# Optimization experiments

Hardware: AMD Instinct MI355X
Metric: run time of the kernel (lower is better)

The kernel has to match this reference:

```python
import jax, jax.numpy as jnp
import numpy as np

NJ = 24
COL = 14
TMP = 3  # gaussian half-window (tmp_size)


def _forward(o, h, o3D, h3D, t, t3D, v):
    B = h.shape[0]
    f32 = jnp.float32
    scale = 1.0 / COL
    cc = COL * COL

    # ---- 2D heatmap argmax decode: x[i,j] = offset at argmax + coord*scale ----
    am = jnp.argmax(h.reshape(B, NJ, cc), axis=-1)            # (B, Nj)
    y2 = am // COL
    x2 = am % COL
    of = o.reshape(B, 2 * NJ, cc)
    gx = jnp.take_along_axis(of[:, :NJ], am[..., None], axis=-1)[..., 0]
    gy = jnp.take_along_axis(of[:, NJ:], am[..., None], axis=-1)[..., 0]
    x2d = jnp.stack([gx + x2.astype(f32) * scale,
                     gy + y2.astype(f32) * scale], axis=-1)   # (B, Nj, 2)

    # ---- 3D heatmap argmax decode ----
    h3r = h3D.reshape(B, NJ, COL, COL, COL)                   # (B, Nj, z, y, x)
    am3 = jnp.argmax(h3r.reshape(B, NJ, COL ** 3), axis=-1)
    z3 = am3 // cc
    r3 = am3 % cc
    y3 = r3 // COL
    x3 = r3 % COL
    o3r = o3D.reshape(B, 3, NJ, COL ** 3)                     # 3 coord channels
    g0 = jnp.take_along_axis(o3r[:, 0], am3[..., None], axis=-1)[..., 0]
    g1 = jnp.take_along_axis(o3r[:, 1], am3[..., None], axis=-1)[..., 0]
    g2 = jnp.take_along_axis(o3r[:, 2], am3[..., None], axis=-1)[..., 0]
    x3d = jnp.stack([g0 + x3.astype(f32) * scale,
                     g1 + y3.astype(f32) * scale,
                     g2 + (z3 - 7).astype(f32) * scale], axis=-1)  # (B, Nj, 3)

    v0 = v[..., 0]
    vis = (v0 == 1)

    # ---- 2D gaussian target placement (torch int() == floor for t >= 0) ----
    mu_x = jnp.floor(t[..., 0] * COL + 0.5).astype(jnp.int32)
    mu_y = jnp.floor(t[..., 1] * COL + 0.5).astype(jnp.int32)
    valid2d = ~((mu_x - TMP >= COL) | (mu_y - TMP >= COL) |
                (mu_x + TMP + 1 <= 0) | (mu_y + TMP + 1 <= 0))
    coords = jnp.arange(COL, dtype=jnp.int32)
    dx = coords[None, None, :] - mu_x[..., None]              # (B, Nj, COL)
    dy = coords[None, None, :] - mu_y[..., None]
    in2 = (jnp.abs(dx) <= TMP)[:, :, None, :] & (jnp.abs(dy) <= TMP)[:, :, :, None]
    sq2 = (dx.astype(f32) ** 2)[:, :, None, :] + (dy.astype(f32) ** 2)[:, :, :, None]
    gate2 = (vis & valid2d)[..., None, None]
    tt = jnp.where(in2 & gate2, jnp.exp(-0.5 * sq2), 0.0)     # (B, Nj, COL, COL)

    # ---- 3D gaussian target placement (only checked when still visible) ----
    m3x = jnp.floor(t3D[..., 0] * COL + 0.5).astype(jnp.int32)
    m3y = jnp.floor(t3D[..., 1] * COL + 0.5).astype(jnp.int32)
    m3z = jnp.floor(t3D[..., 2] * COL + 7 + 0.5).astype(jnp.int32)
    valid3d = ~((m3x - TMP >= COL) | (m3y - TMP >= COL) | (m3z - TMP >= COL) |
                (m3x + TMP + 1 < 0) | (m3y + TMP + 1 < 0) | (m3z + TMP + 1 < 0))
    dX = coords[None, None, :] - m3x[..., None]
    dY = coords[None, None, :] - m3y[..., None]
    dZ = coords[None, None, :] - m3z[..., None]
    in3 = ((jnp.abs(dX) <= TMP)[:, :, None, None, :] &
           (jnp.abs(dY) <= TMP)[:, :, None, :, None] &
           (jnp.abs(dZ) <= TMP)[:, :, :, None, None])
    sq3 = ((dX.astype(f32) ** 2)[:, :, None, None, :] +
           (dY.astype(f32) ** 2)[:, :, None, :, None] +
           (dZ.astype(f32) ** 2)[:, :, :, None, None])
    vf_bool = vis & valid2d & valid3d                          # final visibility
    tt3 = jnp.where(in3 & vf_bool[..., None, None, None], jnp.exp(-0.5 * sq3), 0.0)

    # ---- visibility mutation: v zeroed when a visible joint's target is OOB ----
    keep = jnp.where(vis, valid2d & valid3d, True)
    v_f = v * keep[..., None].astype(f32)                      # (B, Nj, 3)
    # x3D was skipped (left 0) when the 2D check invalidated a visible joint
    x3d = x3d * (~(vis & ~valid2d))[..., None].astype(f32)

    vf0 = v_f[..., 0]
    jmask = (vf0 != 0).astype(f32)                             # (B, Nj)
    cnt = jnp.sum(jmask)
    Nv = jnp.sum(v_f) / 3.0

    diff1 = (h - tt) * jmask[..., None, None]
    d1 = jnp.sqrt(jnp.sum(diff1 * diff1)) / cnt

    diff2 = (x2d - t) * v_f[..., :2]
    d2 = jnp.sqrt(jnp.sum(diff2 * diff2)) / Nv

    diff3 = (h3r - tt3) * jmask[..., None, None, None]
    d3 = jnp.sqrt(jnp.sum(diff3 * diff3)) / cnt

    diff4 = (x3d - t3D) * v_f
    d4 = jnp.sqrt(jnp.sum(diff4 * diff4)) / Nv

    return d1 + d2 + d3 + d4


def setup_inputs() -> dict:
    B = 256
    key = jax.random.key(0)
    ks = jax.random.split(key, 7)
    o = 0.1 * jax.random.normal(ks[0], (B, 2 * NJ, COL, COL), jnp.float32)
    h = jax.random.normal(ks[1], (B, NJ, COL, COL), jnp.float32)
    o3D = 0.1 * jax.random.normal(ks[2], (B, 3 * NJ * COL, COL, COL), jnp.float32)
    h3D = jax.random.normal(ks[3], (B, NJ * COL, COL, COL), jnp.float32)
    t = jax.random.uniform(ks[4], (B, NJ, 2), jnp.float32)
    t3D = jax.random.uniform(ks[5], (B, NJ, 3), jnp.float32)
    v0 = jax.random.bernoulli(ks[6], 0.8, (B, NJ)).astype(jnp.float32)
    v = jnp.repeat(v0[..., None], 3, axis=-1)
    return {"o": o, "h": h, "o3D": o3D, "h3D": h3D, "t": t, "t3D": t3D,
            "v": v, "d": 0, "path": 0}


def reference(o, h, o3D, h3D, t, t3D, v, d, path):
    # d > -990 selects the full d1+d2+d3+d4 loss (static Python branch)
    return _forward(o, h, o3D, h3D, t, t3D, v)
```

## Files before the change

kernel.cpp:

```cpp
#include <hip/hip_runtime.h>
#include <float.h>
#include <math.h>

#define NJ   24
#define COL  14
#define CC   196
#define CC3  2744
#define NV4_3D 686
#define NV4_2D 49
#define TMPW 3
#define PPB  4

__global__ __launch_bounds__(256)
void msed_pair_kernel(const float* __restrict__ o,
                      const float* __restrict__ h,
                      const float* __restrict__ o3D,
                      const float* __restrict__ h3D,
                      const float* __restrict__ t,
                      const float* __restrict__ t3D,
                      const float* __restrict__ v,
                      float* __restrict__ part,
                      int npairs)
{
    const int wv   = threadIdx.x >> 6;
    const int lane = threadIdx.x & 63;
    const int pair = blockIdx.x * PPB + wv;

    __shared__ float warr[PPB][6];

    float p0 = 0.f, p1 = 0.f, p2 = 0.f, p3 = 0.f, p4 = 0.f, p5 = 0.f;

    if (pair < npairs) {
        const float tx  = t[pair * 2 + 0];
        const float ty  = t[pair * 2 + 1];
        const float t3x = t3D[pair * 3 + 0];
        const float t3y = t3D[pair * 3 + 1];
        const float t3z = t3D[pair * 3 + 2];
        const float v0  = v[pair * 3 + 0];
        const float v1  = v[pair * 3 + 1];
        const float v2c = v[pair * 3 + 2];
        const bool vis = (v0 == 1.0f);

        const int mux = (int)floorf(tx * (float)COL + 0.5f);
        const int muy = (int)floorf(ty * (float)COL + 0.5f);
        const bool valid2d = !((mux - TMPW >= COL) || (muy - TMPW >= COL) ||
                               (mux + TMPW + 1 <= 0) || (muy + TMPW + 1 <= 0));

        const int m3x = (int)floorf(t3x * (float)COL + 0.5f);
        const int m3y = (int)floorf(t3y * (float)COL + 0.5f);
        const int m3z = (int)floorf(t3z * (float)COL + 7.0f + 0.5f);
        const bool valid3d = !((m3x - TMPW >= COL) || (m3y - TMPW >= COL) || (m3z - TMPW >= COL) ||
                               (m3x + TMPW + 1 < 0) || (m3y + TMPW + 1 < 0) || (m3z + TMPW + 1 < 0));

        const float keep = vis ? ((valid2d && valid3d) ? 1.0f : 0.0f) : 1.0f;
        const float vf0 = v0 * keep, vf1 = v1 * keep, vf2 = v2c * keep;
        const bool jm     = (vf0 != 0.0f);
        const bool active = jm || (vf1 != 0.0f) || (vf2 != 0.0f);
        const bool gate2  = vis && valid2d;
        const bool gate3  = vis && valid2d && valid3d;

        if (active) {
            const float4* hp3 = (const float4*)(h3D + (size_t)pair * CC3);
            float s3 = 0.0f;
            float bv3 = -FLT_MAX; int bi3 = 0x7FFFFFFF;
            #pragma unroll
            for (int u = 0; u < 11; ++u) {
                const int i = lane + (u << 6);
                const bool valid = (u < 10) || (lane < (NV4_3D - 640));
                const int ic = valid ? i : lane;
                float4 q = hp3[ic];
                float vals[4] = {q.x, q.y, q.z, q.w};
                const int e0 = ic * 4;
                #pragma unroll
                for (int c = 0; c < 4; ++c) {
                    float hv = vals[c];
                    if (valid) {
                        s3 += hv * hv;
                        if (hv > bv3) { bv3 = hv; bi3 = e0 + c; }
                    }
                }
            }

            float s1 = 0.0f;
            float bv2 = -FLT_MAX; int bi2 = 0x7FFFFFFF;
            if (lane < NV4_2D) {
                const float4* hp2 = (const float4*)(h + (size_t)pair * CC);
                float4 q = hp2[lane];
                float vals[4] = {q.x, q.y, q.z, q.w};
                const int e0 = lane * 4;
                #pragma unroll
                for (int c = 0; c < 4; ++c) {
                    float hv = vals[c];
                    s1 += hv * hv;
                    if (hv > bv2) { bv2 = hv; bi2 = e0 + c; }
                }
            }

            if (lane < 49) {
                const int dx = lane % 7 - TMPW;
                const int dy = lane / 7 - TMPW;
                const float gxy = __expf(-0.5f * (float)(dx * dx + dy * dy));

                if (gate2) {
                    const int x = mux + dx, y = muy + dy;
                    if ((unsigned)x < COL && (unsigned)y < COL) {
                        const float wh = h[(size_t)pair * CC + y * COL + x];
                        s1 += gxy * (gxy - 2.0f * wh);
                    }
                }
                if (gate3) {
                    const int x = m3x + dx, y = m3y + dy;
                    if ((unsigned)x < COL && (unsigned)y < COL) {
                        const float* base = h3D + (size_t)pair * CC3 + y * COL + x;
                        #pragma unroll
                        for (int dz = -TMPW; dz <= TMPW; ++dz) {
                            const int z = m3z + dz;
                            if ((unsigned)z < COL) {
                                const float g = gxy * __expf(-0.5f * (float)(dz * dz));
                                const float wh = base[z * CC];
                                s3 += g * (g - 2.0f * wh);
                            }
                        }
                    }
                }
            }

            #pragma unroll
            for (int off = 32; off > 0; off >>= 1) {
                s3 += __shfl_down(s3, off);
                s1 += __shfl_down(s1, off);
                float ov = __shfl_down(bv3, off); int oi = __shfl_down(bi3, off);
                if (ov > bv3 || (ov == bv3 && oi < bi3)) { bv3 = ov; bi3 = oi; }
                float ow = __shfl_down(bv2, off); int oj = __shfl_down(bi2, off);
                if (ow > bv2 || (ow == bv2 && oj < bi2)) { bv2 = ow; bi2 = oj; }
            }

            if (lane == 0) {
                const int b = pair / NJ;
                const int j = pair - b * NJ;
                const float scale = 1.0f / (float)COL;

                const int am = bi2;
                const int x2 = am % COL, y2 = am / COL;
                float gx = o[((size_t)b * (2 * NJ) + j) * CC + am];
                float gy = o[((size_t)b * (2 * NJ) + NJ + j) * CC + am];
                float x2dx = gx + (float)x2 * scale;
                float x2dy = gy + (float)y2 * scale;

                const int am3 = bi3;
                const int z3 = am3 / CC; const int r3 = am3 - z3 * CC;
                const int y3 = r3 / COL; const int x3 = r3 - y3 * COL;
                size_t base3 = (size_t)b * (3 * NJ * CC3) + (size_t)j * CC3 + am3;
                float g0 = o3D[base3];
                float g1 = o3D[base3 + (size_t)NJ * CC3];
                float g2 = o3D[base3 + (size_t)(2 * NJ) * CC3];
                float x3dx = g0 + (float)x3 * scale;
                float x3dy = g1 + (float)y3 * scale;
                float x3dz = g2 + (float)(z3 - 7) * scale;
                if (vis && !valid2d) { x3dx = 0.f; x3dy = 0.f; x3dz = 0.f; }

                float d2x = (x2dx - tx) * vf0;
                float d2y = (x2dy - ty) * vf1;
                float s2 = d2x * d2x + d2y * d2y;

                float d4x = (x3dx - t3x) * vf0;
                float d4y = (x3dy - t3y) * vf1;
                float d4z = (x3dz - t3z) * vf2;
                float s4 = d4x * d4x + d4y * d4y + d4z * d4z;

                p0 = jm ? s1 : 0.f;
                p1 = s2;
                p2 = jm ? s3 : 0.f;
                p3 = s4;
                p4 = jm ? 1.0f : 0.0f;
                p5 = vf0 + vf1 + vf2;
            }
        }
    }

    if (lane == 0) {
        warr[wv][0] = p0; warr[wv][1] = p1; warr[wv][2] = p2;
        warr[wv][3] = p3; warr[wv][4] = p4; warr[wv][5] = p5;
    }
    __syncthreads();

    if (threadIdx.x == 0) {
        float b0 = ((warr[0][0] + warr[1][0]) + warr[2][0]) + warr[3][0];
        float b1 = ((warr[0][1] + warr[1][1]) + warr[2][1]) + warr[3][1];
        float b2 = ((warr[0][2] + warr[1][2]) + warr[2][2]) + warr[3][2];
        float b3 = ((warr[0][3] + warr[1][3]) + warr[2][3]) + warr[3][3];
        float b4 = ((warr[0][4] + warr[1][4]) + warr[2][4]) + warr[3][4];
        float b5 = ((warr[0][5] + warr[1][5]) + warr[2][5]) + warr[3][5];
        *(float4*)(part + (size_t)blockIdx.x * 8)     = make_float4(b0, b1, b2, b3);
        *(float4*)(part + (size_t)blockIdx.x * 8 + 4) = make_float4(b4, b5, 0.f, 0.f);
    }
}

__global__ __launch_bounds__(1024)
void msed_reduce_kernel(const float* __restrict__ part, int nblocks,
                        float* __restrict__ out)
{
    const int tid = threadIdx.x;
    double a0 = 0, a1 = 0, a2 = 0, a3 = 0, a4 = 0, a5 = 0;
    for (int p = tid; p < nblocks; p += 1024) {
        const float4 q0 = *(const float4*)(part + (size_t)p * 8);
        const float4 q1 = *(const float4*)(part + (size_t)p * 8 + 4);
        a0 += (double)q0.x; a1 += (double)q0.y; a2 += (double)q0.z; a3 += (double)q0.w;
        a4 += (double)q1.x; a5 += (double)q1.y;
    }

    #pragma unroll
    for (int off = 32; off > 0; off >>= 1) {
        a0 += __shfl_down(a0, off);
        a1 += __shfl_down(a1, off);
        a2 += __shfl_down(a2, off);
        a3 += __shfl_down(a3, off);
        a4 += __shfl_down(a4, off);
        a5 += __shfl_down(a5, off);
    }

    __shared__ double ws[16][6];
    const int wave = tid >> 6;
    if ((tid & 63) == 0) {
        ws[wave][0] = a0; ws[wave][1] = a1; ws[wave][2] = a2;
        ws[wave][3] = a3; ws[wave][4] = a4; ws[wave][5] = a5;
    }
    __syncthreads();

    if (tid == 0) {
        #pragma unroll
        for (int w = 1; w < 16; ++w) {
            a0 += ws[w][0]; a1 += ws[w][1]; a2 += ws[w][2];
            a3 += ws[w][3]; a4 += ws[w][4]; a5 += ws[w][5];
        }
        double cnt = a4;
        double Nv  = a5 / 3.0;
        float d1 = (float)(sqrt(a0) / cnt);
        float d2 = (float)(sqrt(a1) / Nv);
        float d3 = (float)(sqrt(a2) / cnt);
        float d4 = (float)(sqrt(a3) / Nv);
        out[0] = d1 + d2 + d3 + d4;
    }
}

extern "C" void kernel_launch(void* const* d_in, const int* in_sizes, int n_in,
                              void* d_out, int out_size, void* d_ws, size_t ws_size,
                              hipStream_t stream)
{
    const float* o   = (const float*)d_in[0];
    const float* h   = (const float*)d_in[1];
    const float* o3D = (const float*)d_in[2];
    const float* h3D = (const float*)d_in[3];
    const float* t   = (const float*)d_in[4];
    const float* t3D = (const float*)d_in[5];
    const float* v   = (const float*)d_in[6];

    const int B = in_sizes[1] / (NJ * CC);
    const int npairs  = B * NJ;
    const int nblocks = (npairs + PPB - 1) / PPB;

    float* part = (float*)d_ws;

    msed_pair_kernel<<<nblocks, 256, 0, stream>>>(o, h, o3D, h3D, t, t3D, v, part, npairs);
    msed_reduce_kernel<<<1, 1024, 0, stream>>>(part, nblocks, (float*)d_out);
}
```

Before: 24.05 us.

## Process two joint pairs per wave with all heatmap loads issued upfront

Each wave now handles two (batch, joint) pairs instead of one. All 22 float4 loads of both 3D heatmaps, plus the 2D loads, are issued before any reduction arithmetic. The aim is more memory requests in flight per wave, to hide latency on this bandwidth-bound scan, and half as many blocks. The cost is much higher register pressure from holding the loaded data, which can lower occupancy. Gaussian gating now uses the active flag, which gives the same result because non-visible joints are masked in the epilogue.

```diff
diff --git a/kernel.cpp b/kernel.cpp
--- a/kernel.cpp
+++ b/kernel.cpp
@@ -1,6 +1,7 @@
 #include <hip/hip_runtime.h>
 #include <float.h>
 #include <math.h>
+#include <limits.h>
 
 #define NJ   24
 #define COL  14
@@ -9,7 +10,102 @@
 #define NV4_3D 686
 #define NV4_2D 49
 #define TMPW 3
-#define PPB  4
+#define PPW  2
+#define PPB  8
+
+struct Ctx {
+    bool  active, vis, valid2d, jm;
+    int   mux, muy, m3x, m3y, m3z;
+    float tx, ty, t3x, t3y, t3z, vf0, vf1, vf2;
+};
+
+__device__ __forceinline__ Ctx make_ctx(int pair, int npairs,
+                                        const float* __restrict__ t,
+                                        const float* __restrict__ t3D,
+                                        const float* __restrict__ v)
+{
+    Ctx c;
+    c.active = false; c.jm = false; c.vis = false; c.valid2d = false;
+    c.mux = c.muy = c.m3x = c.m3y = c.m3z = 0;
+    c.tx = c.ty = c.t3x = c.t3y = c.t3z = 0.f;
+    c.vf0 = c.vf1 = c.vf2 = 0.f;
+    if (pair >= npairs) return c;
+
+    c.tx  = t[pair * 2 + 0];
+    c.ty  = t[pair * 2 + 1];
+    c.t3x = t3D[pair * 3 + 0];
+    c.t3y = t3D[pair * 3 + 1];
+    c.t3z = t3D[pair * 3 + 2];
+    const float v0  = v[pair * 3 + 0];
+    const float v1  = v[pair * 3 + 1];
+    const float v2c = v[pair * 3 + 2];
+    c.vis = (v0 == 1.0f);
+
+    c.mux = (int)floorf(c.tx * (float)COL + 0.5f);
+    c.muy = (int)floorf(c.ty * (float)COL + 0.5f);
+    c.valid2d = !((c.mux - TMPW >= COL) || (c.muy - TMPW >= COL) ||
+                  (c.mux + TMPW + 1 <= 0) || (c.muy + TMPW + 1 <= 0));
+
+    c.m3x = (int)floorf(c.t3x * (float)COL + 0.5f);
+    c.m3y = (int)floorf(c.t3y * (float)COL + 0.5f);
+    c.m3z = (int)floorf(c.t3z * (float)COL + 7.0f + 0.5f);
+    const bool valid3d = !((c.m3x - TMPW >= COL) || (c.m3y - TMPW >= COL) || (c.m3z - TMPW >= COL) ||
+                           (c.m3x + TMPW + 1 < 0) || (c.m3y + TMPW + 1 < 0) || (c.m3z + TMPW + 1 < 0));
+
+    const float keep = c.vis ? ((c.valid2d && valid3d) ? 1.0f : 0.0f) : 1.0f;
+    c.vf0 = v0 * keep; c.vf1 = v1 * keep; c.vf2 = v2c * keep;
+    c.jm     = (c.vf0 != 0.0f);
+    c.active = c.jm || (c.vf1 != 0.0f) || (c.vf2 != 0.0f);
+    return c;
+}
+
+__device__ __forceinline__ void epilogue(const Ctx& c, int pair,
+                                         float s1, float s3, int bi2, int bi3,
+                                         const float* __restrict__ o,
+                                         const float* __restrict__ o3D,
+                                         float* __restrict__ p )
+{
+    const bool gate2 = c.vis && c.valid2d;
+    (void)gate2;
+    const int b = pair / NJ;
+    const int j = pair - b * NJ;
+    const float scale = 1.0f / (float)COL;
+
+    const int am = bi2;
+    const int x2 = am % COL, y2 = am / COL;
+    float gx = o[((size_t)b * (2 * NJ) + j) * CC + am];
+    float gy = o[((size_t)b * (2 * NJ) + NJ + j) * CC + am];
+    float x2dx = gx + (float)x2 * scale;
+    float x2dy = gy + (float)y2 * scale;
+
+    const int am3 = bi3;
+    const int z3 = am3 / CC; const int r3 = am3 - z3 * CC;
+    const int y3 = r3 / COL; const int x3 = r3 - y3 * COL;
+    size_t base3 = (size_t)b * (3 * NJ * CC3) + (size_t)j * CC3 + am3;
+    float g0 = o3D[base3];
+    float g1 = o3D[base3 + (size_t)NJ * CC3];
+    float g2 = o3D[base3 + (size_t)(2 * NJ) * CC3];
+    float x3dx = g0 + (float)x3 * scale;
+    float x3dy = g1 + (float)y3 * scale;
+    float x3dz = g2 + (float)(z3 - 7) * scale;
+    if (c.vis && !c.valid2d) { x3dx = 0.f; x3dy = 0.f; x3dz = 0.f; }
+
+    float d2x = (x2dx - c.tx) * c.vf0;
+    float d2y = (x2dy - c.ty) * c.vf1;
+    float s2 = d2x * d2x + d2y * d2y;
+
+    float d4x = (x3dx - c.t3x) * c.vf0;
+    float d4y = (x3dy - c.t3y) * c.vf1;
+    float d4z = (x3dz - c.t3z) * c.vf2;
+    float s4 = d4x * d4x + d4y * d4y + d4z * d4z;
+
+    p[0] = c.jm ? s1 : 0.f;
+    p[1] = s2;
+    p[2] = c.jm ? s3 : 0.f;
+    p[3] = s4;
+    p[4] = c.jm ? 1.0f : 0.0f;
+    p[5] = c.vf0 + c.vf1 + c.vf2;
+}
 
 __global__ __launch_bounds__(256)
 void msed_pair_kernel(const float* __restrict__ o,
@@ -24,163 +120,157 @@
 {
     const int wv   = threadIdx.x >> 6;
     const int lane = threadIdx.x & 63;
-    const int pair = blockIdx.x * PPB + wv;
-
-    __shared__ float warr[PPB][6];
-
-    float p0 = 0.f, p1 = 0.f, p2 = 0.f, p3 = 0.f, p4 = 0.f, p5 = 0.f;
-
-    if (pair < npairs) {
-        const float tx  = t[pair * 2 + 0];
-        const float ty  = t[pair * 2 + 1];
-        const float t3x = t3D[pair * 3 + 0];
-        const float t3y = t3D[pair * 3 + 1];
-        const float t3z = t3D[pair * 3 + 2];
-        const float v0  = v[pair * 3 + 0];
-        const float v1  = v[pair * 3 + 1];
-        const float v2c = v[pair * 3 + 2];
-        const bool vis = (v0 == 1.0f);
-
-        const int mux = (int)floorf(tx * (float)COL + 0.5f);
-        const int muy = (int)floorf(ty * (float)COL + 0.5f);
-        const bool valid2d = !((mux - TMPW >= COL) || (muy - TMPW >= COL) ||
-                               (mux + TMPW + 1 <= 0) || (muy + TMPW + 1 <= 0));
-
-        const int m3x = (int)floorf(t3x * (float)COL + 0.5f);
-        const int m3y = (int)floorf(t3y * (float)COL + 0.5f);
-        const int m3z = (int)floorf(t3z * (float)COL + 7.0f + 0.5f);
-        const bool valid3d = !((m3x - TMPW >= COL) || (m3y - TMPW >= COL) || (m3z - TMPW >= COL) ||
-                               (m3x + TMPW + 1 < 0) || (m3y + TMPW + 1 < 0) || (m3z + TMPW + 1 < 0));
-
-        const float keep = vis ? ((valid2d && valid3d) ? 1.0f : 0.0f) : 1.0f;
-        const float vf0 = v0 * keep, vf1 = v1 * keep, vf2 = v2c * keep;
-        const bool jm     = (vf0 != 0.0f);
-        const bool active = jm || (vf1 != 0.0f) || (vf2 != 0.0f);
-        const bool gate2  = vis && valid2d;
-        const bool gate3  = vis && valid2d && valid3d;
-
-        if (active) {
-            const float4* hp3 = (const float4*)(h3D + (size_t)pair * CC3);
-            float s3 = 0.0f;
-            float bv3 = -FLT_MAX; int bi3 = 0x7FFFFFFF;
-            #pragma unroll
-            for (int u = 0; u < 11; ++u) {
-                const int i = lane + (u << 6);
-                const bool valid = (u < 10) || (lane < (NV4_3D - 640));
-                const int ic = valid ? i : lane;
-                float4 q = hp3[ic];
-                float vals[4] = {q.x, q.y, q.z, q.w};
-                const int e0 = ic * 4;
+    const int pairA = blockIdx.x * PPB + wv * PPW;
+    const int pairB = pairA + 1;
+
+    __shared__ float warr[4][6];
+
+    const Ctx cA = make_ctx(pairA, npairs, t, t3D, v);
+    const Ctx cB = make_ctx(pairB, npairs, t, t3D, v);
+
+    float4 qa[11], qb[11];
+    const bool tailOk = lane < (NV4_3D - 640);
+    if (cA.active) {
+        const float4* hp = (const float4*)(h3D + (size_t)pairA * CC3);
+        #pragma unroll
+        for (int u = 0; u < 11; ++u) {
+            const int i = lane + (u << 6);
+            qa[u] = hp[(u < 10 || tailOk) ? i : lane];
+        }
+    }
+    if (cB.active) {
+        const float4* hp = (const float4*)(h3D + (size_t)pairB * CC3);
+        #pragma unroll
+        for (int u = 0; u < 11; ++u) {
+            const int i = lane + (u << 6);
+            qb[u] = hp[(u < 10 || tailOk) ? i : lane];
+        }
+    }
+    float4 q2a = make_float4(0.f,0.f,0.f,0.f), q2b = make_float4(0.f,0.f,0.f,0.f);
+    if (cA.active && lane < NV4_2D) q2a = ((const float4*)(h + (size_t)pairA * CC))[lane];
+    if (cB.active && lane < NV4_2D) q2b = ((const float4*)(h + (size_t)pairB * CC))[lane];
+
+    float s3a = 0.f, s3b = 0.f, s1a = 0.f, s1b = 0.f;
+    float bv3a = -FLT_MAX, bv3b = -FLT_MAX, bv2a = -FLT_MAX, bv2b = -FLT_MAX;
+    int   bi3a = INT_MAX, bi3b = INT_MAX, bi2a = INT_MAX, bi2b = INT_MAX;
+
+    if (cA.active) {
+        #pragma unroll
+        for (int u = 0; u < 11; ++u) {
+            if (u < 10 || tailOk) {
+                const int e0 = (lane + (u << 6)) * 4;
+                float vals[4] = {qa[u].x, qa[u].y, qa[u].z, qa[u].w};
                 #pragma unroll
                 for (int c = 0; c < 4; ++c) {
                     float hv = vals[c];
-                    if (valid) {
-                        s3 += hv * hv;
-                        if (hv > bv3) { bv3 = hv; bi3 = e0 + c; }
-                    }
+                    s3a += hv * hv;
+                    if (hv > bv3a) { bv3a = hv; bi3a = e0 + c; }
                 }
             }
-
-            float s1 = 0.0f;
-            float bv2 = -FLT_MAX; int bi2 = 0x7FFFFFFF;
-            if (lane < NV4_2D) {
-                const float4* hp2 = (const float4*)(h + (size_t)pair * CC);
-                float4 q = hp2[lane];
-                float vals[4] = {q.x, q.y, q.z, q.w};
-                const int e0 = lane * 4;
+        }
+        if (lane < NV4_2D) {
+            float vals[4] = {q2a.x, q2a.y, q2a.z, q2a.w};
+            #pragma unroll
+            for (int c = 0; c < 4; ++c) {
+                float hv = vals[c];
+                s1a += hv * hv;
+                if (hv > bv2a) { bv2a = hv; bi2a = lane * 4 + c; }
+            }
+        }
+    }
+    if (cB.active) {
+        #pragma unroll
+        for (int u = 0; u < 11; ++u) {
+            if (u < 10 || tailOk) {
+                const int e0 = (lane + (u << 6)) * 4;
+                float vals[4] = {qb[u].x, qb[u].y, qb[u].z, qb[u].w};
                 #pragma unroll
                 for (int c = 0; c < 4; ++c) {
                     float hv = vals[c];
-                    s1 += hv * hv;
-                    if (hv > bv2) { bv2 = hv; bi2 = e0 + c; }
+                    s3b += hv * hv;
+                    if (hv > bv3b) { bv3b = hv; bi3b = e0 + c; }
                 }
             }
-
-            if (lane < 49) {
-                const int dx = lane % 7 - TMPW;
-                const int dy = lane / 7 - TMPW;
-                const float gxy = __expf(-0.5f * (float)(dx * dx + dy * dy));
-
-                if (gate2) {
-                    const int x = mux + dx, y = muy + dy;
-                    if ((unsigned)x < COL && (unsigned)y < COL) {
-                        const float wh = h[(size_t)pair * CC + y * COL + x];
-                        s1 += gxy * (gxy - 2.0f * wh);
+        }
+        if (lane < NV4_2D) {
+            float vals[4] = {q2b.x, q2b.y, q2b.z, q2b.w};
+            #pragma unroll
+            for (int c = 0; c < 4; ++c) {
+                float hv = vals[c];
+                s1b += hv * hv;
+                if (hv > bv2b) { bv2b = hv; bi2b = lane * 4 + c; }
+            }
+        }
+    }
+
+    if (lane < 49) {
+        const int dx = lane % 7 - TMPW;
+        const int dy = lane / 7 - TMPW;
+        const float gxy = __expf(-0.5f * (float)(dx * dx + dy * dy));
+
+        if (cA.active) {
+            const int x = cA.mux + dx, y = cA.muy + dy;
+            if ((unsigned)x < COL && (unsigned)y < COL) {
+                const float wh = h[(size_t)pairA * CC + y * COL + x];
+                s1a += gxy * (gxy - 2.0f * wh);
+            }
+            const int x3 = cA.m3x + dx, y3 = cA.m3y + dy;
+            if ((unsigned)x3 < COL && (unsigned)y3 < COL) {
+                const float* base = h3D + (size_t)pairA * CC3 + y3 * COL + x3;
+                #pragma unroll
+                for (int dz = -TMPW; dz <= TMPW; ++dz) {
+                    const int z = cA.m3z + dz;
+                    if ((unsigned)z < COL) {
+                        const float g = gxy * __expf(-0.5f * (float)(dz * dz));
+                        s3a += g * (g - 2.0f * base[z * CC]);
                     }
                 }
-                if (gate3) {
-                    const int x = m3x + dx, y = m3y + dy;
-                    if ((unsigned)x < COL && (unsigned)y < COL) {
-                        const float* base = h3D + (size_t)pair * CC3 + y * COL + x;
-                        #pragma unroll
-                        for (int dz = -TMPW; dz <= TMPW; ++dz) {
-                            const int z = m3z + dz;
-                            if ((unsigned)z < COL) {
-                                const float g = gxy * __expf(-0.5f * (float)(dz * dz));
-                                const float wh = base[z * CC];
-                                s3 += g * (g - 2.0f * wh);
-                            }
-                        }
+            }
+        }
+        if (cB.active) {
+            const int x = cB.mux + dx, y = cB.muy + dy;
+            if ((unsigned)x < COL && (unsigned)y < COL) {
+                const float wh = h[(size_t)pairB * CC + y * COL + x];
+                s1b += gxy * (gxy - 2.0f * wh);
+            }
+            const int x3 = cB.m3x + dx, y3 = cB.m3y + dy;
+            if ((unsigned)x3 < COL && (unsigned)y3 < COL) {
+                const float* base = h3D + (size_t)pairB * CC3 + y3 * COL + x3;
+                #pragma unroll
+                for (int dz = -TMPW; dz <= TMPW; ++dz) {
+                    const int z = cB.m3z + dz;
+                    if ((unsigned)z < COL) {
+                        const float g = gxy * __expf(-0.5f * (float)(dz * dz));
+                        s3b += g * (g - 2.0f * base[z * CC]);
                     }
                 }
             }
-
-            #pragma unroll
-            for (int off = 32; off > 0; off >>= 1) {
-                s3 += __shfl_down(s3, off);
-                s1 += __shfl_down(s1, off);
-                float ov = __shfl_down(bv3, off); int oi = __shfl_down(bi3, off);
-                if (ov > bv3 || (ov == bv3 && oi < bi3)) { bv3 = ov; bi3 = oi; }
-                float ow = __shfl_down(bv2, off); int oj = __shfl_down(bi2, off);
-                if (ow > bv2 || (ow == bv2 && oj < bi2)) { bv2 = ow; bi2 = oj; }
-            }
-
-            if (lane == 0) {
-                const int b = pair / NJ;
-                const int j = pair - b * NJ;
-                const float scale = 1.0f / (float)COL;
-
-                const int am = bi2;
-                const int x2 = am % COL, y2 = am / COL;
-                float gx = o[((size_t)b * (2 * NJ) + j) * CC + am];
-                float gy = o[((size_t)b * (2 * NJ) + NJ + j) * CC + am];
-                float x2dx = gx + (float)x2 * scale;
-                float x2dy = gy + (float)y2 * scale;
-
-                const int am3 = bi3;
-                const int z3 = am3 / CC; const int r3 = am3 - z3 * CC;
-                const int y3 = r3 / COL; const int x3 = r3 - y3 * COL;
-                size_t base3 = (size_t)b * (3 * NJ * CC3) + (size_t)j * CC3 + am3;
-                float g0 = o3D[base3];
-                float g1 = o3D[base3 + (size_t)NJ * CC3];
-                float g2 = o3D[base3 + (size_t)(2 * NJ) * CC3];
-                float x3dx = g0 + (float)x3 * scale;
-                float x3dy = g1 + (float)y3 * scale;
-                float x3dz = g2 + (float)(z3 - 7) * scale;
-                if (vis && !valid2d) { x3dx = 0.f; x3dy = 0.f; x3dz = 0.f; }
-
-                float d2x = (x2dx - tx) * vf0;
-                float d2y = (x2dy - ty) * vf1;
-                float s2 = d2x * d2x + d2y * d2y;
-
-                float d4x = (x3dx - t3x) * vf0;
-                float d4y = (x3dy - t3y) * vf1;
-                float d4z = (x3dz - t3z) * vf2;
-                float s4 = d4x * d4x + d4y * d4y + d4z * d4z;
-
-                p0 = jm ? s1 : 0.f;
-                p1 = s2;
-                p2 = jm ? s3 : 0.f;
-                p3 = s4;
-                p4 = jm ? 1.0f : 0.0f;
-                p5 = vf0 + vf1 + vf2;
-            }
-        }
+        }
+    }
+
+    #pragma unroll
+    for (int off = 32; off > 0; off >>= 1) {
+        s3a += __shfl_down(s3a, off);
+        s1a += __shfl_down(s1a, off);
+        s3b += __shfl_down(s3b, off);
+        s1b += __shfl_down(s1b, off);
+        float ov; int oi;
+        ov = __shfl_down(bv3a, off); oi = __shfl_down(bi3a, off);
+        if (ov > bv3a || (ov == bv3a && oi < bi3a)) { bv3a = ov; bi3a = oi; }
+        ov = __shfl_down(bv2a, off); oi = __shfl_down(bi2a, off);
+        if (ov > bv2a || (ov == bv2a && oi < bi2a)) { bv2a = ov; bi2a = oi; }
+        ov = __shfl_down(bv3b, off); oi = __shfl_down(bi3b, off);
+        if (ov > bv3b || (ov == bv3b && oi < bi3b)) { bv3b = ov; bi3b = oi; }
+        ov = __shfl_down(bv2b, off); oi = __shfl_down(bi2b, off);
+        if (ov > bv2b || (ov == bv2b && oi < bi2b)) { bv2b = ov; bi2b = oi; }
     }
 
     if (lane == 0) {
-        warr[wv][0] = p0; warr[wv][1] = p1; warr[wv][2] = p2;
-        warr[wv][3] = p3; warr[wv][4] = p4; warr[wv][5] = p5;
+        float pa[6] = {0,0,0,0,0,0}, pb[6] = {0,0,0,0,0,0};
+        if (cA.active) epilogue(cA, pairA, s1a, s3a, bi2a, bi3a, o, o3D, pa);
+        if (cB.active) epilogue(cB, pairB, s1b, s3b, bi2b, bi3b, o, o3D, pb);
+        #pragma unroll
+        for (int k = 0; k < 6; ++k) warr[wv][k] = pa[k] + pb[k];
     }
     __syncthreads();
 
@@ -197,12 +287,12 @@
 }
 
 __global__ __launch_bounds__(1024)
-void msed_reduce_kernel(const float* __restrict__ part, int nblocks,
+void msed_reduce_kernel(const float* __restrict__ part, int nparts,
                         float* __restrict__ out)
 {
     const int tid = threadIdx.x;
     double a0 = 0, a1 = 0, a2 = 0, a3 = 0, a4 = 0, a5 = 0;
-    for (int p = tid; p < nblocks; p += 1024) {
+    for (int p = tid; p < nparts; p += 1024) {
         const float4 q0 = *(const float4*)(part + (size_t)p * 8);
         const float4 q1 = *(const float4*)(part + (size_t)p * 8 + 4);
         a0 += (double)q0.x; a1 += (double)q0.y; a2 += (double)q0.z; a3 += (double)q0.w;
```

Result: no change. 24.30 us (+1.0%).
